# Performance work log

Measured on AMD Instinct MI355X. Metric: run time of the kernel, lower is better.

## Reference

```python
import jax, jax.numpy as jnp
import numpy as np

B, DIN, H, DOUT, NC = 1024, 343, 512, 311, 4


def cubic(y0, y1, y2, y3, mu):
    # Catmull-Rom cubic interpolation (matches PFNN.cubic)
    return ((-0.5 * y0 + 1.5 * y1 - 1.5 * y2 + 0.5 * y3) * mu * mu * mu
            + (y0 - 2.5 * y1 + 2.0 * y2 - 0.5 * y3) * mu * mu
            + (-0.5 * y0 + 0.5 * y2) * mu + y1)


def setup_inputs() -> dict:
    key = jax.random.key(0)
    ks = jax.random.split(key, 7)
    s = 0.05
    x = jax.random.uniform(ks[0], (B, DIN), dtype=jnp.float32)  # phase = x[:, -1] in [0,1)
    W0 = jax.random.normal(ks[1], (NC, H, DIN - 1), dtype=jnp.float32) * s
    W1 = jax.random.normal(ks[2], (NC, H, H), dtype=jnp.float32) * s
    W2 = jax.random.normal(ks[3], (NC, DOUT, H), dtype=jnp.float32) * s
    b0 = jax.random.normal(ks[4], (NC, H), dtype=jnp.float32) * s
    b1 = jax.random.normal(ks[5], (NC, H), dtype=jnp.float32) * s
    b2 = jax.random.normal(ks[6], (NC, DOUT), dtype=jnp.float32) * s
    return {"x": x, "W0": W0, "W1": W1, "W2": W2, "b0": b0, "b1": b1, "b2": b2}


def reference(x, W0, W1, W2, b0, b1, b2):
    nc = W0.shape[0]
    phase = x[:, -1]                       # [B]
    pscale = nc * phase
    mu = jnp.mod(pscale, 1.0)              # [B]
    k1 = jnp.mod(pscale.astype(jnp.int32), nc)
    k0 = jnp.mod(k1 - 1, nc)
    k2 = jnp.mod(k1 + 1, nc)
    k3 = jnp.mod(k1 + 2, nc)
    muW = mu[:, None, None]
    mub = mu[:, None]

    def interp(P, m):
        return cubic(P[k0], P[k1], P[k2], P[k3], m)

    W0i = interp(W0, muW)  # [B, 512, DIN-1]
    W1i = interp(W1, muW)  # [B, 512, 512]
    W2i = interp(W2, muW)  # [B, DOUT, 512]
    b0i = interp(b0, mub)
    b1i = interp(b1, mub)
    b2i = interp(b2, mub)

    h0 = x[:, :-1]                                              # [B, DIN-1]
    h1 = jax.nn.elu(jnp.einsum('boi,bi->bo', W0i, h0) + b0i)    # [B, 512]
    h2 = jax.nn.elu(jnp.einsum('boi,bi->bo', W1i, h1) + b1i)    # [B, 512]
    h3 = jnp.einsum('boi,bi->bo', W2i, h2) + b2i                # [B, DOUT]
    return h3
```

## Files before the change

### kernel.cpp

```cpp
#include <hip/hip_runtime.h>
#include <math.h>

typedef short bf16x8 __attribute__((ext_vector_type(8)));
typedef float f32x16 __attribute__((ext_vector_type(16)));

__device__ __forceinline__ unsigned short f2bf(float f) {
    union { float f; unsigned u; } x; x.f = f;
    unsigned r = x.u + 0x7FFFu + ((x.u >> 16) & 1u);
    return (unsigned short)(r >> 16);
}

template<int NKS_T>
__device__ void transpose_tile(const float* __restrict__ W, const float* __restrict__ bias,
                               int rowbase, int rowlimit, int Kreal, int ldsrc,
                               unsigned short* __restrict__ dst, float* s, int tid)
{
    constexpr int NCHK = NKS_T / 4;
    const int r = tid >> 3, l = tid & 7;
    const int ks_l = tid >> 6, lane = tid & 63;
    const int m = lane & 31, h = lane >> 5;
    for (int kc = 0; kc < NCHK; ++kc) {
        {
            int kb = kc * 64 + l * 8;
            const bool rv = r < rowlimit;
            const float* src = W + (size_t)(rowbase + r) * ldsrc + kb;
            float v[8];
            if (rv && kb + 7 < Kreal) {
                #pragma unroll
                for (int i = 0; i < 8; ++i) v[i] = src[i];
            } else {
                #pragma unroll
                for (int i = 0; i < 8; ++i) {
                    int k = kb + i;
                    v[i] = (rv && k < Kreal) ? src[i]
                         : ((rv && k == Kreal) ? (bias ? bias[rowbase + r] : 1.0f) : 0.f);
                }
            }
            #pragma unroll
            for (int i = 0; i < 8; ++i) s[r * 66 + l * 8 + i] = v[i];
        }
        __syncthreads();
        {
            bf16x8 pk;
            #pragma unroll
            for (int j = 0; j < 8; ++j)
                pk[j] = (short)f2bf(s[m * 66 + ks_l * 16 + h * 8 + j]);
            *(bf16x8*)(dst + ((size_t)(kc * 4 + ks_l) * 64 + lane) * 8) = pk;
        }
        __syncthreads();
    }
}

__global__ void __launch_bounds__(256) phaseA_kernel(
    const float* __restrict__ x,
    const float* __restrict__ W0, const float* __restrict__ W1, const float* __restrict__ W2,
    const float* __restrict__ bias0, const float* __restrict__ bias1, const float* __restrict__ bias2,
    float* __restrict__ coef, unsigned short* __restrict__ xf,
    unsigned short* __restrict__ H1f, unsigned short* __restrict__ H2f,
    unsigned short* __restrict__ Wf0, unsigned short* __restrict__ Wf1, unsigned short* __restrict__ Wf2)
{
    __shared__ float s[32 * 66];
    const int bid = blockIdx.x, tid = threadIdx.x;

    if (bid < 32) {
        const int bt = bid;
        if (tid < 32) {
            int b = bt * 32 + tid;
            float phase = x[(size_t)b * 343 + 342];
            float ps = 4.0f * phase;
            int k1 = (int)ps;
            float mu = ps - (float)k1;
            k1 &= 3;
            float mu2 = mu * mu, mu3 = mu2 * mu;
            float c0 = -0.5f * mu3 +        mu2 - 0.5f * mu;
            float c1 =  1.5f * mu3 - 2.5f * mu2 + 1.0f;
            float c2 = -1.5f * mu3 + 2.0f * mu2 + 0.5f * mu;
            float c3 =  0.5f * mu3 - 0.5f * mu2;
            float cc[4];
            cc[(k1 + 3) & 3] = c0;
            cc[k1]           = c1;
            cc[(k1 + 1) & 3] = c2;
            cc[(k1 + 2) & 3] = c3;
            *(float4*)(coef + b * 4) = make_float4(cc[0], cc[1], cc[2], cc[3]);
        }
        {
            int kk = tid >> 6, lane = tid & 63;
            size_t off = ((size_t)(bt * 36 + 32 + kk) * 64 + lane) * 8;
            bf16x8 v;
            #pragma unroll
            for (int j = 0; j < 8; ++j)
                v[j] = (short)((kk == 0 && (lane >> 5) == 0 && j == 0) ? 0x3F80 : 0);
            *(bf16x8*)(H1f + off) = v;
            *(bf16x8*)(H2f + off) = v;
        }
        transpose_tile<24>(x, nullptr, bt * 32, 32, 342, 343,
                           xf + (size_t)bt * 24 * 512, s, tid);
    } else if (bid < 96) {
        int idx = bid - 32, n = idx >> 4, ot = idx & 15;
        transpose_tile<24>(W0, bias0, n * 512 + ot * 32, 32, 342, 342,
                           Wf0 + (size_t)(n * 16 + ot) * 24 * 512, s, tid);
    } else if (bid < 160) {
        int idx = bid - 96, n = idx >> 4, ot = idx & 15;
        transpose_tile<36>(W1, bias1, n * 512 + ot * 32, 32, 512, 512,
                           Wf1 + (size_t)(n * 16 + ot) * 36 * 512, s, tid);
    } else {
        int idx = bid - 160, n = idx / 10, ot = idx % 10;
        int rl = 311 - ot * 32; if (rl > 32) rl = 32;
        transpose_tile<36>(W2, bias2, n * 311 + ot * 32, rl, 512, 512,
                           Wf2 + (size_t)(n * 10 + ot) * 36 * 512, s, tid);
    }
}

template<bool ELU, bool OUT_BF16, int KP, int OPAD>
__device__ __forceinline__ void layer_phase(
    const unsigned short* __restrict__ Wf,
    const unsigned short* __restrict__ Hf,
    const float* __restrict__ coef,
    unsigned short* __restrict__ HoutF,
    float* __restrict__ outF, int Oreal,
    float* red, int bid, int tid)
{
    constexpr int NOT = OPAD / 32, NKS = KP / 16, KSQ = NKS / 4;
    constexpr int CH = 3, NC2 = KSQ / CH;
    const int lane = tid & 63, w = tid >> 6;
    const int m = lane & 31, h = lane >> 5;
    const size_t nstr = (size_t)NOT * NKS * 512;

    const int ot = bid >> 5, bt = bid & 31;
    const unsigned short* wbase = Wf + ((size_t)ot * NKS + w * KSQ) * 512 + (size_t)lane * 8;
    const unsigned short* bbase = Hf + ((size_t)bt * NKS + w * KSQ) * 512 + (size_t)lane * 8;

    f32x16 acc0 = {}, acc1 = {}, acc2 = {}, acc3 = {};
    bf16x8 Ab[2][CH][4], Bb[2][CH];

    #pragma unroll
    for (int sI = 0; sI < CH; ++sI) {
        Bb[0][sI] = *(const bf16x8*)(bbase + (size_t)sI * 512);
        #pragma unroll
        for (int n = 0; n < 4; ++n)
            Ab[0][sI][n] = *(const bf16x8*)(wbase + (size_t)n * nstr + (size_t)sI * 512);
    }
    #pragma unroll
    for (int c = 0; c < NC2; ++c) {
        const int cur = c & 1;
        if (c + 1 < NC2) {
            const int nxt = cur ^ 1;
            #pragma unroll
            for (int sI = 0; sI < CH; ++sI) {
                int st = (c + 1) * CH + sI;
                Bb[nxt][sI] = *(const bf16x8*)(bbase + (size_t)st * 512);
                #pragma unroll
                for (int n = 0; n < 4; ++n)
                    Ab[nxt][sI][n] = *(const bf16x8*)(wbase + (size_t)n * nstr + (size_t)st * 512);
            }
        }
        #pragma unroll
        for (int sI = 0; sI < CH; ++sI) {
            acc0 = __builtin_amdgcn_mfma_f32_32x32x16_bf16(Ab[cur][sI][0], Bb[cur][sI], acc0, 0, 0, 0);
            acc1 = __builtin_amdgcn_mfma_f32_32x32x16_bf16(Ab[cur][sI][1], Bb[cur][sI], acc1, 0, 0, 0);
            acc2 = __builtin_amdgcn_mfma_f32_32x32x16_bf16(Ab[cur][sI][2], Bb[cur][sI], acc2, 0, 0, 0);
            acc3 = __builtin_amdgcn_mfma_f32_32x32x16_bf16(Ab[cur][sI][3], Bb[cur][sI], acc3, 0, 0, 0);
        }
    }

    const int b = bt * 32 + m;
    float4 cf = *(const float4*)(coef + b * 4);
    #pragma unroll
    for (int g = 0; g < 4; ++g)
        #pragma unroll
        for (int j = 0; j < 4; ++j) {
            int rI = g * 4 + j;
            float v = cf.x * acc0[rI] + cf.y * acc1[rI] + cf.z * acc2[rI] + cf.w * acc3[rI];
            red[w * 1024 + (8 * g + 4 * h + j) * 32 + m] = v;
        }
    __syncthreads();
    {
        float vv[4];
        #pragma unroll
        for (int j = 0; j < 4; ++j) {
            int row = 8 * w + 4 * h + j;
            float v = red[row * 32 + m] + red[1024 + row * 32 + m]
                    + red[2048 + row * 32 + m] + red[3072 + row * 32 + m];
            if (ELU) v = (v > 0.f) ? v : expm1f(v);
            vv[j] = v;
        }
        if (OUT_BF16) {
            size_t off = (((size_t)bt * 36 + ot * 2 + (w >> 1)) * 64
                          + (w & 1) * 32 + m) * 8 + 4 * h;
            ushort4 pk;
            pk.x = f2bf(vv[0]); pk.y = f2bf(vv[1]); pk.z = f2bf(vv[2]); pk.w = f2bf(vv[3]);
            *(ushort4*)(HoutF + off) = pk;
        } else {
            int orow = ot * 32 + 8 * w + 4 * h;
            #pragma unroll
            for (int j = 0; j < 4; ++j)
                if (orow + j < Oreal) outF[(size_t)b * Oreal + orow + j] = vv[j];
        }
    }
}

__global__ void __launch_bounds__(256, 2) layer0_kernel(
    const unsigned short* __restrict__ Wf0, const unsigned short* __restrict__ xf,
    const float* __restrict__ coef, unsigned short* __restrict__ H1f)
{
    __shared__ float red[4 * 1024];
    layer_phase<true, true, 384, 512>(Wf0, xf, coef, H1f, nullptr, 512,
                                      red, blockIdx.x, threadIdx.x);
}
__global__ void __launch_bounds__(256, 2) layer1_kernel(
    const unsigned short* __restrict__ Wf1, const unsigned short* __restrict__ H1f,
    const float* __restrict__ coef, unsigned short* __restrict__ H2f)
{
    __shared__ float red[4 * 1024];
    layer_phase<true, true, 576, 512>(Wf1, H1f, coef, H2f, nullptr, 512,
                                      red, blockIdx.x, threadIdx.x);
}
__global__ void __launch_bounds__(256, 2) layer2_kernel(
    const unsigned short* __restrict__ Wf2, const unsigned short* __restrict__ H2f,
    const float* __restrict__ coef, float* __restrict__ outF)
{
    __shared__ float red[4 * 1024];
    layer_phase<false, false, 576, 320>(Wf2, H2f, coef, nullptr, outF, 311,
                                        red, blockIdx.x, threadIdx.x);
}

extern "C" void kernel_launch(void* const* d_in, const int* in_sizes, int n_in,
                              void* d_out, int out_size, void* d_ws, size_t ws_size,
                              hipStream_t stream) {
    (void)in_sizes; (void)n_in; (void)out_size; (void)ws_size;
    const float* x  = (const float*)d_in[0];
    const float* W0 = (const float*)d_in[1];
    const float* W1 = (const float*)d_in[2];
    const float* W2 = (const float*)d_in[3];
    const float* b0 = (const float*)d_in[4];
    const float* b1 = (const float*)d_in[5];
    const float* b2 = (const float*)d_in[6];
    float* out = (float*)d_out;

    char* wsb = (char*)d_ws;
    float*          coef = (float*)(wsb + 0);
    unsigned short* xf   = (unsigned short*)(wsb + 16384);
    unsigned short* H1f  = (unsigned short*)(wsb + 802816);
    unsigned short* H2f  = (unsigned short*)(wsb + 1982464);
    unsigned short* Wf0  = (unsigned short*)(wsb + 3162112);
    unsigned short* Wf1  = (unsigned short*)(wsb + 4734976);
    unsigned short* Wf2  = (unsigned short*)(wsb + 7094272);

    phaseA_kernel<<<dim3(200), dim3(256), 0, stream>>>(
        x, W0, W1, W2, b0, b1, b2, coef, xf, H1f, H2f, Wf0, Wf1, Wf2);
    layer0_kernel<<<dim3(512), dim3(256), 0, stream>>>(Wf0, xf,  coef, H1f);
    layer1_kernel<<<dim3(512), dim3(256), 0, stream>>>(Wf1, H1f, coef, H2f);
    layer2_kernel<<<dim3(320), dim3(256), 0, stream>>>(Wf2, H2f, coef, out);
}
```

Measured before the change: 94.91 us.

## Fuse four kernel launches into one cooperative persistent kernel with grid barriers

Merges the weight/input transpose phase and the three MLP layer phases into a single cooperative kernel. The phases are separated by a software grid barrier built from atomic counters, and each phase uses grid-stride loops over its tiles. The aim is to remove the launch gaps and tail idle time between four dependent launches. In exchange it adds barrier spin overhead and a memset of the barrier words, and it relies on the cooperative launch succeeding, falling back to the original four launches otherwise.

```diff
diff --git a/kernel.cpp b/kernel.cpp
--- a/kernel.cpp
+++ b/kernel.cpp
@@ -8,6 +8,23 @@
     union { float f; unsigned u; } x; x.f = f;
     unsigned r = x.u + 0x7FFFu + ((x.u >> 16) & 1u);
     return (unsigned short)(r >> 16);
+}
+
+__device__ __forceinline__ void grid_barrier(unsigned* cnt, unsigned* gen, unsigned nblk) {
+    __syncthreads();
+    if (threadIdx.x == 0) {
+        __threadfence();
+        unsigned g = __hip_atomic_load(gen, __ATOMIC_RELAXED, __HIP_MEMORY_SCOPE_AGENT);
+        if (__hip_atomic_fetch_add(cnt, 1u, __ATOMIC_ACQ_REL, __HIP_MEMORY_SCOPE_AGENT) == nblk - 1u) {
+            __hip_atomic_store(cnt, 0u, __ATOMIC_RELAXED, __HIP_MEMORY_SCOPE_AGENT);
+            __hip_atomic_fetch_add(gen, 1u, __ATOMIC_RELEASE, __HIP_MEMORY_SCOPE_AGENT);
+        } else {
+            while (__hip_atomic_load(gen, __ATOMIC_ACQUIRE, __HIP_MEMORY_SCOPE_AGENT) == g)
+                __builtin_amdgcn_s_sleep(2);
+        }
+        (void)__hip_atomic_load(gen, __ATOMIC_ACQUIRE, __HIP_MEMORY_SCOPE_AGENT);
+    }
+    __syncthreads();
 }
 
 template<int NKS_T>
@@ -51,7 +68,8 @@
     }
 }
 
-__global__ void __launch_bounds__(256) phaseA_kernel(
+__device__ void phaseA_unit(
+    int u, int tid, float* s,
     const float* __restrict__ x,
     const float* __restrict__ W0, const float* __restrict__ W1, const float* __restrict__ W2,
     const float* __restrict__ bias0, const float* __restrict__ bias1, const float* __restrict__ bias2,
@@ -59,11 +77,8 @@
     unsigned short* __restrict__ H1f, unsigned short* __restrict__ H2f,
     unsigned short* __restrict__ Wf0, unsigned short* __restrict__ Wf1, unsigned short* __restrict__ Wf2)
 {
-    __shared__ float s[32 * 66];
-    const int bid = blockIdx.x, tid = threadIdx.x;
-
-    if (bid < 32) {
-        const int bt = bid;
+    if (u < 32) {
+        const int bt = u;
         if (tid < 32) {
             int b = bt * 32 + tid;
             float phase = x[(size_t)b * 343 + 342];
@@ -95,16 +110,16 @@
         }
         transpose_tile<24>(x, nullptr, bt * 32, 32, 342, 343,
                            xf + (size_t)bt * 24 * 512, s, tid);
-    } else if (bid < 96) {
-        int idx = bid - 32, n = idx >> 4, ot = idx & 15;
+    } else if (u < 96) {
+        int idx = u - 32, n = idx >> 4, ot = idx & 15;
         transpose_tile<24>(W0, bias0, n * 512 + ot * 32, 32, 342, 342,
                            Wf0 + (size_t)(n * 16 + ot) * 24 * 512, s, tid);
-    } else if (bid < 160) {
-        int idx = bid - 96, n = idx >> 4, ot = idx & 15;
+    } else if (u < 160) {
+        int idx = u - 96, n = idx >> 4, ot = idx & 15;
         transpose_tile<36>(W1, bias1, n * 512 + ot * 32, 32, 512, 512,
                            Wf1 + (size_t)(n * 16 + ot) * 36 * 512, s, tid);
     } else {
-        int idx = bid - 160, n = idx / 10, ot = idx % 10;
+        int idx = u - 160, n = idx / 10, ot = idx % 10;
         int rl = 311 - ot * 32; if (rl > 32) rl = 32;
         transpose_tile<36>(W2, bias2, n * 311 + ot * 32, rl, 512, 512,
                            Wf2 + (size_t)(n * 10 + ot) * 36 * 512, s, tid);
@@ -118,7 +133,7 @@
     const float* __restrict__ coef,
     unsigned short* __restrict__ HoutF,
     float* __restrict__ outF, int Oreal,
-    float* red, int bid, int tid)
+    float* red, int bid, int tid, int gdim)
 {
     constexpr int NOT = OPAD / 32, NKS = KP / 16, KSQ = NKS / 4;
     constexpr int CH = 3, NC2 = KSQ / CH;
@@ -126,102 +141,128 @@
     const int m = lane & 31, h = lane >> 5;
     const size_t nstr = (size_t)NOT * NKS * 512;
 
-    const int ot = bid >> 5, bt = bid & 31;
-    const unsigned short* wbase = Wf + ((size_t)ot * NKS + w * KSQ) * 512 + (size_t)lane * 8;
-    const unsigned short* bbase = Hf + ((size_t)bt * NKS + w * KSQ) * 512 + (size_t)lane * 8;
-
-    f32x16 acc0 = {}, acc1 = {}, acc2 = {}, acc3 = {};
-    bf16x8 Ab[2][CH][4], Bb[2][CH];
-
-    #pragma unroll
-    for (int sI = 0; sI < CH; ++sI) {
-        Bb[0][sI] = *(const bf16x8*)(bbase + (size_t)sI * 512);
-        #pragma unroll
-        for (int n = 0; n < 4; ++n)
-            Ab[0][sI][n] = *(const bf16x8*)(wbase + (size_t)n * nstr + (size_t)sI * 512);
-    }
-    #pragma unroll
-    for (int c = 0; c < NC2; ++c) {
-        const int cur = c & 1;
-        if (c + 1 < NC2) {
-            const int nxt = cur ^ 1;
-            #pragma unroll
-            for (int sI = 0; sI < CH; ++sI) {
-                int st = (c + 1) * CH + sI;
-                Bb[nxt][sI] = *(const bf16x8*)(bbase + (size_t)st * 512);
-                #pragma unroll
-                for (int n = 0; n < 4; ++n)
-                    Ab[nxt][sI][n] = *(const bf16x8*)(wbase + (size_t)n * nstr + (size_t)st * 512);
-            }
-        }
+    for (int t = bid; t < NOT * 32; t += gdim) {
+        const int ot = t >> 5, bt = t & 31;
+        const unsigned short* wbase = Wf + ((size_t)ot * NKS + w * KSQ) * 512 + (size_t)lane * 8;
+        const unsigned short* bbase = Hf + ((size_t)bt * NKS + w * KSQ) * 512 + (size_t)lane * 8;
+
+        f32x16 acc0 = {}, acc1 = {}, acc2 = {}, acc3 = {};
+        bf16x8 Ab[2][CH][4], Bb[2][CH];
+
         #pragma unroll
         for (int sI = 0; sI < CH; ++sI) {
-            acc0 = __builtin_amdgcn_mfma_f32_32x32x16_bf16(Ab[cur][sI][0], Bb[cur][sI], acc0, 0, 0, 0);
-            acc1 = __builtin_amdgcn_mfma_f32_32x32x16_bf16(Ab[cur][sI][1], Bb[cur][sI], acc1, 0, 0, 0);
-            acc2 = __builtin_amdgcn_mfma_f32_32x32x16_bf16(Ab[cur][sI][2], Bb[cur][sI], acc2, 0, 0, 0);
-            acc3 = __builtin_amdgcn_mfma_f32_32x32x16_bf16(Ab[cur][sI][3], Bb[cur][sI], acc3, 0, 0, 0);
-        }
-    }
-
-    const int b = bt * 32 + m;
-    float4 cf = *(const float4*)(coef + b * 4);
-    #pragma unroll
-    for (int g = 0; g < 4; ++g)
+            Bb[0][sI] = *(const bf16x8*)(bbase + (size_t)sI * 512);
+            #pragma unroll
+            for (int n = 0; n < 4; ++n)
+                Ab[0][sI][n] = *(const bf16x8*)(wbase + (size_t)n * nstr + (size_t)sI * 512);
+        }
         #pragma unroll
-        for (int j = 0; j < 4; ++j) {
-            int rI = g * 4 + j;
-            float v = cf.x * acc0[rI] + cf.y * acc1[rI] + cf.z * acc2[rI] + cf.w * acc3[rI];
-            red[w * 1024 + (8 * g + 4 * h + j) * 32 + m] = v;
-        }
-    __syncthreads();
-    {
-        float vv[4];
+        for (int c = 0; c < NC2; ++c) {
+            const int cur = c & 1;
+            if (c + 1 < NC2) {
+                const int nxt = cur ^ 1;
+                #pragma unroll
+                for (int sI = 0; sI < CH; ++sI) {
+                    int st = (c + 1) * CH + sI;
+                    Bb[nxt][sI] = *(const bf16x8*)(bbase + (size_t)st * 512);
+                    #pragma unroll
+                    for (int n = 0; n < 4; ++n)
+                        Ab[nxt][sI][n] = *(const bf16x8*)(wbase + (size_t)n * nstr + (size_t)st * 512);
+                }
+            }
+            #pragma unroll
+            for (int sI = 0; sI < CH; ++sI) {
+                acc0 = __builtin_amdgcn_mfma_f32_32x32x16_bf16(Ab[cur][sI][0], Bb[cur][sI], acc0, 0, 0, 0);
+                acc1 = __builtin_amdgcn_mfma_f32_32x32x16_bf16(Ab[cur][sI][1], Bb[cur][sI], acc1, 0, 0, 0);
+                acc2 = __builtin_amdgcn_mfma_f32_32x32x16_bf16(Ab[cur][sI][2], Bb[cur][sI], acc2, 0, 0, 0);
+                acc3 = __builtin_amdgcn_mfma_f32_32x32x16_bf16(Ab[cur][sI][3], Bb[cur][sI], acc3, 0, 0, 0);
+            }
+        }
+
+        const int b = bt * 32 + m;
+        float4 cf = *(const float4*)(coef + b * 4);
         #pragma unroll
-        for (int j = 0; j < 4; ++j) {
-            int row = 8 * w + 4 * h + j;
-            float v = red[row * 32 + m] + red[1024 + row * 32 + m]
-                    + red[2048 + row * 32 + m] + red[3072 + row * 32 + m];
-            if (ELU) v = (v > 0.f) ? v : expm1f(v);
-            vv[j] = v;
-        }
-        if (OUT_BF16) {
-            size_t off = (((size_t)bt * 36 + ot * 2 + (w >> 1)) * 64
-                          + (w & 1) * 32 + m) * 8 + 4 * h;
-            ushort4 pk;
-            pk.x = f2bf(vv[0]); pk.y = f2bf(vv[1]); pk.z = f2bf(vv[2]); pk.w = f2bf(vv[3]);
-            *(ushort4*)(HoutF + off) = pk;
-        } else {
-            int orow = ot * 32 + 8 * w + 4 * h;
-            #pragma unroll
-            for (int j = 0; j < 4; ++j)
-                if (orow + j < Oreal) outF[(size_t)b * Oreal + orow + j] = vv[j];
-        }
-    }
-}
-
-__global__ void __launch_bounds__(256, 2) layer0_kernel(
-    const unsigned short* __restrict__ Wf0, const unsigned short* __restrict__ xf,
-    const float* __restrict__ coef, unsigned short* __restrict__ H1f)
-{
+        for (int g = 0; g < 4; ++g)
+            #pragma unroll
+            for (int j = 0; j < 4; ++j) {
+                int rI = g * 4 + j;
+                float v = cf.x * acc0[rI] + cf.y * acc1[rI] + cf.z * acc2[rI] + cf.w * acc3[rI];
+                red[w * 1024 + (8 * g + 4 * h + j) * 32 + m] = v;
+            }
+        __syncthreads();
+        {
+            float vv[4];
+            #pragma unroll
+            for (int j = 0; j < 4; ++j) {
+                int row = 8 * w + 4 * h + j;
+                float v = red[row * 32 + m] + red[1024 + row * 32 + m]
+                        + red[2048 + row * 32 + m] + red[3072 + row * 32 + m];
+                if (ELU) v = (v > 0.f) ? v : expm1f(v);
+                vv[j] = v;
+            }
+            if (OUT_BF16) {
+                size_t off = (((size_t)bt * 36 + ot * 2 + (w >> 1)) * 64
+                              + (w & 1) * 32 + m) * 8 + 4 * h;
+                ushort4 pk;
+                pk.x = f2bf(vv[0]); pk.y = f2bf(vv[1]); pk.z = f2bf(vv[2]); pk.w = f2bf(vv[3]);
+                *(ushort4*)(HoutF + off) = pk;
+            } else {
+                int orow = ot * 32 + 8 * w + 4 * h;
+                #pragma unroll
+                for (int j = 0; j < 4; ++j)
+                    if (orow + j < Oreal) outF[(size_t)b * Oreal + orow + j] = vv[j];
+            }
+        }
+        __syncthreads();
+    }
+}
+
+#define PFNN_PARAMS \
+    const float* __restrict__ x, \
+    const float* __restrict__ W0, const float* __restrict__ W1, const float* __restrict__ W2, \
+    const float* __restrict__ bias0, const float* __restrict__ bias1, const float* __restrict__ bias2, \
+    float* __restrict__ outF, float* __restrict__ coef, \
+    unsigned short* __restrict__ xf, \
+    unsigned short* __restrict__ H1f, unsigned short* __restrict__ H2f, \
+    unsigned short* __restrict__ Wf0, unsigned short* __restrict__ Wf1, unsigned short* __restrict__ Wf2
+
+__global__ void __launch_bounds__(256, 2) pfnn_fused(PFNN_PARAMS, unsigned* bar, unsigned nblk) {
+    __shared__ union { float s[32 * 66]; float red[4 * 1024]; } u;
+    const int bid = blockIdx.x, tid = threadIdx.x, gdim = gridDim.x;
+    unsigned* cnt = bar;
+    unsigned* gen = bar + 16;
+
+    for (int un = bid; un < 200; un += gdim)
+        phaseA_unit(un, tid, u.s, x, W0, W1, W2, bias0, bias1, bias2,
+                    coef, xf, H1f, H2f, Wf0, Wf1, Wf2);
+    grid_barrier(cnt, gen, nblk);
+    layer_phase<true,  true,  384, 512>(Wf0, xf,  coef, H1f, nullptr, 512, u.red, bid, tid, gdim);
+    grid_barrier(cnt, gen, nblk);
+    layer_phase<true,  true,  576, 512>(Wf1, H1f, coef, H2f, nullptr, 512, u.red, bid, tid, gdim);
+    grid_barrier(cnt, gen, nblk);
+    layer_phase<false, false, 576, 320>(Wf2, H2f, coef, nullptr, outF, 311, u.red, bid, tid, gdim);
+}
+
+__global__ void __launch_bounds__(256) phaseA_kernel(PFNN_PARAMS) {
+    __shared__ float s[32 * 66];
+    for (int un = blockIdx.x; un < 200; un += gridDim.x)
+        phaseA_unit(un, threadIdx.x, s, x, W0, W1, W2, bias0, bias1, bias2,
+                    coef, xf, H1f, H2f, Wf0, Wf1, Wf2);
+    (void)outF;
+}
+__global__ void __launch_bounds__(256, 2) layer0_kernel(PFNN_PARAMS) {
     __shared__ float red[4 * 1024];
-    layer_phase<true, true, 384, 512>(Wf0, xf, coef, H1f, nullptr, 512,
-                                      red, blockIdx.x, threadIdx.x);
-}
-__global__ void __launch_bounds__(256, 2) layer1_kernel(
-    const unsigned short* __restrict__ Wf1, const unsigned short* __restrict__ H1f,
-    const float* __restrict__ coef, unsigned short* __restrict__ H2f)
-{
+    layer_phase<true, true, 384, 512>(Wf0, xf, coef, H1f, nullptr, 512, red, blockIdx.x, threadIdx.x, gridDim.x);
+    (void)outF;
+}
+__global__ void __launch_bounds__(256, 2) layer1_kernel(PFNN_PARAMS) {
     __shared__ float red[4 * 1024];
-    layer_phase<true, true, 576, 512>(Wf1, H1f, coef, H2f, nullptr, 512,
-                                      red, blockIdx.x, threadIdx.x);
-}
-__global__ void __launch_bounds__(256, 2) layer2_kernel(
-    const unsigned short* __restrict__ Wf2, const unsigned short* __restrict__ H2f,
-    const float* __restrict__ coef, float* __restrict__ outF)
-{
+    layer_phase<true, true, 576, 512>(Wf1, H1f, coef, H2f, nullptr, 512, red, blockIdx.x, threadIdx.x, gridDim.x);
+    (void)outF;
+}
+__global__ void __launch_bounds__(256, 2) layer2_kernel(PFNN_PARAMS) {
     __shared__ float red[4 * 1024];
-    layer_phase<false, false, 576, 320>(Wf2, H2f, coef, nullptr, outF, 311,
-                                        red, blockIdx.x, threadIdx.x);
+    layer_phase<false, false, 576, 320>(Wf2, H2f, coef, nullptr, outF, 311, red, blockIdx.x, threadIdx.x, gridDim.x);
 }
 
 extern "C" void kernel_launch(void* const* d_in, const int* in_sizes, int n_in,
@@ -245,10 +286,30 @@
     unsigned short* Wf0  = (unsigned short*)(wsb + 3162112);
     unsigned short* Wf1  = (unsigned short*)(wsb + 4734976);
     unsigned short* Wf2  = (unsigned short*)(wsb + 7094272);
-
-    phaseA_kernel<<<dim3(200), dim3(256), 0, stream>>>(
-        x, W0, W1, W2, b0, b1, b2, coef, xf, H1f, H2f, Wf0, Wf1, Wf2);
-    layer0_kernel<<<dim3(512), dim3(256), 0, stream>>>(Wf0, xf,  coef, H1f);
-    layer1_kernel<<<dim3(512), dim3(256), 0, stream>>>(Wf1, H1f, coef, H2f);
-    layer2_kernel<<<dim3(320), dim3(256), 0, stream>>>(Wf2, H2f, coef, out);
-}
+    unsigned*       bar  = (unsigned*)(wsb + 8568832);
+
+    int maxb = 0;
+    hipError_t qe = hipOccupancyMaxActiveBlocksPerMultiprocessor(
+        &maxb, (const void*)pfnn_fused, 256, 0);
+    unsigned grid = 256;
+    if (qe == hipSuccess && maxb >= 2) grid = 512;
+
+    hipMemsetAsync(bar, 0, 128, stream);
+
+    void* args[] = {
+        (void*)&x, (void*)&W0, (void*)&W1, (void*)&W2,
+        (void*)&b0, (void*)&b1, (void*)&b2, (void*)&out,
+        (void*)&coef, (void*)&xf, (void*)&H1f, (void*)&H2f,
+        (void*)&Wf0, (void*)&Wf1, (void*)&Wf2,
+        (void*)&bar, (void*)&grid
+    };
+    hipError_t e = hipLaunchCooperativeKernel((const void*)pfnn_fused,
+                                              dim3(grid), dim3(256), args, 0, stream);
+    if (e != hipSuccess) {
+        (void)hipGetLastError();
+        phaseA_kernel<<<dim3(200), dim3(256), 0, stream>>>(x, W0, W1, W2, b0, b1, b2, out, coef, xf, H1f, H2f, Wf0, Wf1, Wf2);
+        layer0_kernel<<<dim3(512), dim3(256), 0, stream>>>(x, W0, W1, W2, b0, b1, b2, out, coef, xf, H1f, H2f, Wf0, Wf1, Wf2);
+        layer1_kernel<<<dim3(512), dim3(256), 0, stream>>>(x, W0, W1, W2, b0, b1, b2, out, coef, xf, H1f, H2f, Wf0, Wf1, Wf2);
+        layer2_kernel<<<dim3(320), dim3(256), 0, stream>>>(x, W0, W1, W2, b0, b1, b2, out, coef, xf, H1f, H2f, Wf0, Wf1, Wf2);
+    }
+}
```

Result: slower. 323.1 us (+240.4%).
